# Performance work log

Measured on AMD Instinct MI355X. Metric: run time of the kernel, lower is better.

Reference implementation:

```python
import jax, jax.numpy as jnp
import numpy as np

N_NODES = 50000


def gcn_conv(x, src, dst, W, b, n_nodes):
    """PyG-style GCNConv: x' = D^-1/2 (A + I) D^-1/2 (x W) + b.
    src/dst already include self-loops."""
    h = x @ W  # [N, C_out]
    # symmetric normalization from degree (with self-loops, unit edge weight)
    deg = jax.ops.segment_sum(jnp.ones_like(dst, dtype=h.dtype), dst,
                              num_segments=n_nodes)  # [N]
    dinv = jnp.where(deg > 0, jax.lax.rsqrt(deg), 0.0)
    norm = dinv[src] * dinv[dst]  # [E]
    msg = h[src] * norm[:, None]  # gather + scale, [E, C_out]
    out = jax.ops.segment_sum(msg, dst, num_segments=n_nodes)  # scatter-add
    return out + b


def setup_inputs() -> dict:
    key = jax.random.key(0)
    k1, k2, k3, k4, k5, k6 = jax.random.split(key, 6)
    in_c, hid_c, out_c = 128, 64, 64
    x = jax.random.normal(k1, (N_NODES, in_c), dtype=jnp.float32)
    edge_index = jax.random.randint(k2, (2, 800000), 0, N_NODES, dtype=jnp.int64)
    # Glorot-ish init for weights, zeros for bias (as PyG default)
    W1 = jax.random.normal(k3, (in_c, hid_c), dtype=jnp.float32) / np.sqrt(in_c)
    b1 = jnp.zeros((hid_c,), dtype=jnp.float32)
    W2 = jax.random.normal(k4, (hid_c, out_c), dtype=jnp.float32) / np.sqrt(hid_c)
    b2 = jnp.zeros((out_c,), dtype=jnp.float32)
    return {"x": x, "edge_index": edge_index, "W1": W1, "b1": b1,
            "W2": W2, "b2": b2}


def reference(x, edge_index, W1, b1, W2, b2):
    n = x.shape[0]
    loops = jnp.arange(n, dtype=edge_index.dtype)
    src = jnp.concatenate([edge_index[0], loops])  # add self-loops
    dst = jnp.concatenate([edge_index[1], loops])
    h = gcn_conv(x, src, dst, W1, b1, n)
    h = jax.nn.relu(h)
    return gcn_conv(h, src, dst, W2, b2, n)
```

## Files before the change

kernel.cpp:

```cpp
#include <hip/hip_runtime.h>
#include <hip/hip_fp16.h>


#define C_HID 64
#define NCHUNK 512
#define ES3 1280
#define ES4 768

static inline size_t alignup(size_t x) { return (x + 255) & ~(size_t)255; }

typedef __attribute__((address_space(3))) unsigned int lds_uint;
typedef __attribute__((address_space(1))) const unsigned int glob_uint;

__device__ __forceinline__ int blockScanIncl256(int v, int* wsum) {
    const int lane = threadIdx.x & 63, wav = threadIdx.x >> 6;
    int s = v;
#pragma unroll
    for (int off = 1; off < 64; off <<= 1) {
        int t = __shfl_up(s, off);
        if (lane >= off) s += t;
    }
    if (lane == 63) wsum[wav] = s;
    __syncthreads();
    if (wav == 0 && lane < 4) {
        int ws = wsum[lane];
#pragma unroll
        for (int off = 1; off < 4; off <<= 1) {
            int t = __shfl_up(ws, off);
            if (lane >= off) ws += t;
        }
        wsum[lane] = ws;
    }
    __syncthreads();
    return (wav ? wsum[wav - 1] : 0) + s;
}

template <int K>
__global__ __launch_bounds__(256) void gemm1_hist_kernel(
    const float* __restrict__ X, const float* __restrict__ W,
    const int* __restrict__ dst, __half* __restrict__ outh,
    int* __restrict__ S, int n, int E, int ePer, int nb) {
    constexpr int KP = K + 4;
    __shared__ float Xs[64 * KP];
    __shared__ float Ws[K * 64];
    __shared__ int h[1024];
    const int t = threadIdx.x;
    const int lane = t & 63;
    const int wav = t >> 6;

    if ((int)blockIdx.x < NCHUNK) {
        for (int i = t; i < nb; i += 256) h[i] = 0;
        __syncthreads();
        int beg = blockIdx.x * ePer, end = min(E, beg + ePer);
        for (int e = beg + t; e < end; e += 256)
            atomicAdd(&h[dst[e] >> 6], 1);
        __syncthreads();
        for (int b = t; b < nb; b += 256)
            S[(size_t)b * NCHUNK + blockIdx.x] = h[b];
        return;
    }

    const int row0 = ((int)blockIdx.x - NCHUNK) * 64;
    {
        const char* gb = (const char*)W;
        char* lb = (char*)Ws;
        for (int off = wav * 1024; off < K * 64 * 4; off += 4096)
            __builtin_amdgcn_global_load_lds((glob_uint*)(gb + off + lane * 16),
                                             (lds_uint*)(lb + off), 16, 0, 0);
    }
    if (row0 + 64 <= n) {
        const float4* g4 = (const float4*)(X + (size_t)row0 * K);
        for (int i = t; i < 64 * (K / 4); i += 256) {
            float4 v = g4[i];
            int r = i / (K / 4), k0 = (i % (K / 4)) * 4;
            *(float4*)&Xs[r * KP + k0] = v;
        }
    } else {
        for (int i = t; i < 64 * K; i += 256) {
            int r = i / K, k = i % K;
            Xs[r * KP + k] = (row0 + r < n) ? X[(size_t)(row0 + r) * K + k] : 0.0f;
        }
    }
    __syncthreads();

    const int tx = t & 15;
    const int ty = t >> 4;
    float acc[4][4] = {{0.f}};
#pragma unroll 2
    for (int k0 = 0; k0 < K; k0 += 4) {
        float4 a0 = *(const float4*)&Xs[(4 * ty + 0) * KP + k0];
        float4 a1 = *(const float4*)&Xs[(4 * ty + 1) * KP + k0];
        float4 a2 = *(const float4*)&Xs[(4 * ty + 2) * KP + k0];
        float4 a3 = *(const float4*)&Xs[(4 * ty + 3) * KP + k0];
        float4 b0 = *(const float4*)&Ws[(k0 + 0) * 64 + 4 * tx];
        float4 b1 = *(const float4*)&Ws[(k0 + 1) * 64 + 4 * tx];
        float4 b2 = *(const float4*)&Ws[(k0 + 2) * 64 + 4 * tx];
        float4 b3 = *(const float4*)&Ws[(k0 + 3) * 64 + 4 * tx];
        const float* ap[4] = {(const float*)&a0, (const float*)&a1,
                              (const float*)&a2, (const float*)&a3};
        const float* bp[4] = {(const float*)&b0, (const float*)&b1,
                              (const float*)&b2, (const float*)&b3};
#pragma unroll
        for (int r = 0; r < 4; ++r)
#pragma unroll
            for (int kk = 0; kk < 4; ++kk) {
                float av = ap[r][kk];
#pragma unroll
                for (int c = 0; c < 4; ++c)
                    acc[r][c] = fmaf(av, bp[kk][c], acc[r][c]);
            }
    }
#pragma unroll
    for (int r = 0; r < 4; ++r) {
        int row = row0 + 4 * ty + r;
        if (row < n) {
            __half2 p01 = __floats2half2_rn(acc[r][0], acc[r][1]);
            __half2 p23 = __floats2half2_rn(acc[r][2], acc[r][3]);
            float2 st;
            ((__half2*)&st)[0] = p01;
            ((__half2*)&st)[1] = p23;
            *(float2*)&outh[(size_t)row * 64 + 4 * tx] = st;
        }
    }
}

__global__ __launch_bounds__(256) void scan_rows_kernel(
    int* __restrict__ S, int* __restrict__ T) {
    __shared__ int wsum[4];
    const int b = blockIdx.x, t = threadIdx.x;
    int4 v = make_int4(0, 0, 0, 0);
    if (t < NCHUNK / 4) v = ((const int4*)(S + (size_t)b * NCHUNK))[t];
    int p1 = v.x + v.y, p2 = p1 + v.z, p3 = p2 + v.w;
    int incl = blockScanIncl256(p3, wsum);
    int excl = incl - p3;
    if (t < NCHUNK / 4) {
        int4 o;
        o.x = excl; o.y = excl + v.x; o.z = excl + p1; o.w = excl + p2;
        ((int4*)(S + (size_t)b * NCHUNK))[t] = o;
    }
    if (t == 0) T[b] = wsum[3];
}

__global__ __launch_bounds__(256) void scatter_kernel(
    const int* __restrict__ src, const int* __restrict__ dst, int E, int ePer,
    const int* __restrict__ S, const int* __restrict__ T,
    unsigned* __restrict__ ebuf, int nb) {
    __shared__ int tmp[1024];
    __shared__ int arr[1024];
    __shared__ int wsum[4];
    const int b = blockIdx.x, t = threadIdx.x;
    {
        int a0 = (4 * t + 0 < nb) ? T[4 * t + 0] : 0;
        int a1 = (4 * t + 1 < nb) ? T[4 * t + 1] : 0;
        int a2 = (4 * t + 2 < nb) ? T[4 * t + 2] : 0;
        int a3 = (4 * t + 3 < nb) ? T[4 * t + 3] : 0;
        int p1 = a0 + a1, p2 = p1 + a2, p3 = p2 + a3;
        int incl = blockScanIncl256(p3, wsum);
        int excl = incl - p3;
        tmp[4 * t + 0] = excl;
        tmp[4 * t + 1] = excl + a0;
        tmp[4 * t + 2] = excl + p1;
        tmp[4 * t + 3] = excl + p2;
    }
    __syncthreads();
    for (int i = t; i < nb; i += 256)
        arr[i] = S[(size_t)i * NCHUNK + b] + tmp[i];
    __syncthreads();
    int beg = b * ePer, end = min(E, beg + ePer);
    for (int e = beg + t; e < end; e += 256) {
        int d = dst[e];
        int s = src[e];
        int pos = atomicAdd(&arr[d >> 6], 1);
        ebuf[pos] = ((unsigned)s << 6) | (unsigned)(d & 63);
    }
}

__global__ __launch_bounds__(256) void build_kernel(
    const unsigned* __restrict__ ebuf, const int* __restrict__ T,
    int* __restrict__ row_ptr, float* __restrict__ dinv,
    int* __restrict__ esrc, __half* __restrict__ g1, int n, int nb) {
    __shared__ int tmp[1024];
    __shared__ int cnt[64];
    __shared__ int cur[64];
    __shared__ float dvs[64];
    __shared__ int wsum[4];
    const int b = blockIdx.x, t = threadIdx.x;
    {
        int a0 = (4 * t + 0 < nb) ? T[4 * t + 0] : 0;
        int a1 = (4 * t + 1 < nb) ? T[4 * t + 1] : 0;
        int a2 = (4 * t + 2 < nb) ? T[4 * t + 2] : 0;
        int a3 = (4 * t + 3 < nb) ? T[4 * t + 3] : 0;
        int p1 = a0 + a1, p2 = p1 + a2, p3 = p2 + a3;
        int incl = blockScanIncl256(p3, wsum);
        int excl = incl - p3;
        tmp[4 * t + 0] = excl + a0;
        tmp[4 * t + 1] = excl + p1;
        tmp[4 * t + 2] = excl + p2;
        tmp[4 * t + 3] = excl + p3;
    }
    if (t < 64) cnt[t] = 0;
    __syncthreads();
    const int ebeg = b ? tmp[b - 1] : 0;
    const int eend = tmp[b];

    for (int e = ebeg + t; e < eend; e += 256)
        atomicAdd(&cnt[ebuf[e] & 63], 1);
    __syncthreads();
    if (t < 64) {
        int deg = cnt[t];
        int s = deg;
#pragma unroll
        for (int off = 1; off < 64; off <<= 1) {
            int x = __shfl_up(s, off);
            if (t >= off) s += x;
        }
        cur[t] = ebeg + s - deg;
        float dv = rsqrtf(1.0f + (float)deg);
        dvs[t] = dv;
        int v = (b << 6) + t;
        if (v < n) {
            row_ptr[v + 1] = ebeg + s;
            dinv[v] = dv;
            if (v == 0) row_ptr[0] = 0;
        }
    }
    __syncthreads();
    for (int e = ebeg + t; e < eend; e += 256) {
        unsigned p = ebuf[e];
        int pos = atomicAdd(&cur[p & 63], 1);
        esrc[pos] = (int)(p >> 6);
    }
    {
        const int row = t >> 2, q = t & 3;
        const int v = (b << 6) + row;
        if (v < n) {
            float dv = dvs[row];
            float4* gp = (float4*)(g1 + (size_t)v * 64 + q * 16);
            float4 r0 = gp[0], r1 = gp[1];
            __half2* h0 = (__half2*)&r0;
            __half2* h1 = (__half2*)&r1;
#pragma unroll
            for (int i2 = 0; i2 < 4; ++i2) {
                float2 f0 = __half22float2(h0[i2]);
                float2 f1 = __half22float2(h1[i2]);
                h0[i2] = __floats2half2_rn(f0.x * dv, f0.y * dv);
                h1[i2] = __floats2half2_rn(f1.x * dv, f1.y * dv);
            }
            gp[0] = r0;
            gp[1] = r1;
        }
    }
}

template <bool LDSE>
__device__ __forceinline__ void agg1_body(
    const float4* __restrict__ hs4, const int* es, const int* __restrict__ esg,
    int beg0, int beg, int end, int c, float acc[16]) {
    int j = beg;
    for (; j + 4 <= end; j += 4) {
        int s0, s1, s2, s3;
        if (LDSE) {
            s0 = es[j]; s1 = es[j + 1]; s2 = es[j + 2]; s3 = es[j + 3];
        } else {
            s0 = esg[beg0 + j]; s1 = esg[beg0 + j + 1];
            s2 = esg[beg0 + j + 2]; s3 = esg[beg0 + j + 3];
        }
        size_t rb0 = (size_t)s0 * 8 + 2 * c, rb1 = (size_t)s1 * 8 + 2 * c;
        size_t rb2 = (size_t)s2 * 8 + 2 * c, rb3 = (size_t)s3 * 8 + 2 * c;
        float4 a0 = hs4[rb0], a1 = hs4[rb0 + 1];
        float4 b0 = hs4[rb1], b1v = hs4[rb1 + 1];
        float4 c0 = hs4[rb2], c1 = hs4[rb2 + 1];
        float4 e0 = hs4[rb3], e1 = hs4[rb3 + 1];
        const __half2 *pa0 = (const __half2*)&a0, *pa1 = (const __half2*)&a1;
        const __half2 *pb0 = (const __half2*)&b0, *pb1 = (const __half2*)&b1v;
        const __half2 *pc0 = (const __half2*)&c0, *pc1 = (const __half2*)&c1;
        const __half2 *pe0 = (const __half2*)&e0, *pe1 = (const __half2*)&e1;
#pragma unroll
        for (int q = 0; q < 4; ++q) {
            float2 f;
            f = __half22float2(pa0[q]); acc[2 * q] += f.x; acc[2 * q + 1] += f.y;
            f = __half22float2(pa1[q]); acc[8 + 2 * q] += f.x; acc[9 + 2 * q] += f.y;
            f = __half22float2(pb0[q]); acc[2 * q] += f.x; acc[2 * q + 1] += f.y;
            f = __half22float2(pb1[q]); acc[8 + 2 * q] += f.x; acc[9 + 2 * q] += f.y;
            f = __half22float2(pc0[q]); acc[2 * q] += f.x; acc[2 * q + 1] += f.y;
            f = __half22float2(pc1[q]); acc[8 + 2 * q] += f.x; acc[9 + 2 * q] += f.y;
            f = __half22float2(pe0[q]); acc[2 * q] += f.x; acc[2 * q + 1] += f.y;
            f = __half22float2(pe1[q]); acc[8 + 2 * q] += f.x; acc[9 + 2 * q] += f.y;
        }
    }
    for (; j < end; ++j) {
        int s0 = LDSE ? es[j] : esg[beg0 + j];
        size_t rb0 = (size_t)s0 * 8 + 2 * c;
        float4 a0 = hs4[rb0], a1 = hs4[rb0 + 1];
        const __half2 *pa0 = (const __half2*)&a0, *pa1 = (const __half2*)&a1;
#pragma unroll
        for (int q = 0; q < 4; ++q) {
            float2 f;
            f = __half22float2(pa0[q]); acc[2 * q] += f.x; acc[2 * q + 1] += f.y;
            f = __half22float2(pa1[q]); acc[8 + 2 * q] += f.x; acc[9 + 2 * q] += f.y;
        }
    }
}

__global__ __launch_bounds__(256) void agg1_gemm2_kernel(
    const __half* __restrict__ g1, const int* __restrict__ row_ptr,
    const int* __restrict__ esrc, const float* __restrict__ dinv,
    const float* __restrict__ b1, const float* __restrict__ W2,
    __half* __restrict__ g2, int n) {
    __shared__ float Bt[64][68];
    __shared__ float Ws2[64 * 64];
    __shared__ int es[ES3];
    const int t = threadIdx.x, lane = t & 63, wav = t >> 6;
    const int row0 = blockIdx.x * 64;

    const int beg0 = row_ptr[row0];
    const int end0 = row_ptr[min(row0 + 64, n)];
    const int tot = end0 - beg0;
    const bool uselds = (tot <= ES3);
    if (uselds)
        for (int i = t; i < tot; i += 256) es[i] = esrc[beg0 + i];
    __syncthreads();

    {
        const char* gb = (const char*)W2;
        char* lb = (char*)Ws2;
        for (int off = wav * 1024; off < 64 * 64 * 4; off += 4096)
            __builtin_amdgcn_global_load_lds((glob_uint*)(gb + off + lane * 16),
                                             (lds_uint*)(lb + off), 16, 0, 0);
    }

    const int g = t >> 2;
    const int c = t & 3;
    const int v = row0 + g;
    const float4* __restrict__ hs4 = (const float4*)g1;

    if (v < n) {
        float acc[16];
        {
            size_t rb = (size_t)v * 8 + 2 * c;
            float4 r0 = hs4[rb], r1 = hs4[rb + 1];
            const __half2* h0 = (const __half2*)&r0;
            const __half2* h1 = (const __half2*)&r1;
#pragma unroll
            for (int q = 0; q < 4; ++q) {
                float2 f0 = __half22float2(h0[q]);
                float2 f1 = __half22float2(h1[q]);
                acc[2 * q] = f0.x;     acc[2 * q + 1] = f0.y;
                acc[8 + 2 * q] = f1.x; acc[9 + 2 * q] = f1.y;
            }
        }
        const int beg = row_ptr[v] - beg0;
        const int end = row_ptr[v + 1] - beg0;
        if (uselds) agg1_body<true>(hs4, es, esrc, beg0, beg, end, c, acc);
        else        agg1_body<false>(hs4, es, esrc, beg0, beg, end, c, acc);
        const float dv0 = dinv[v];
        const float* bb = b1 + c * 16;
#pragma unroll
        for (int u = 0; u < 4; ++u) {
            float4 w;
            w.x = fmaxf(fmaf(acc[4 * u + 0], dv0, bb[4 * u + 0]), 0.f);
            w.y = fmaxf(fmaf(acc[4 * u + 1], dv0, bb[4 * u + 1]), 0.f);
            w.z = fmaxf(fmaf(acc[4 * u + 2], dv0, bb[4 * u + 2]), 0.f);
            w.w = fmaxf(fmaf(acc[4 * u + 3], dv0, bb[4 * u + 3]), 0.f);
            *(float4*)&Bt[g][c * 16 + 4 * u] = w;
        }
    } else {
#pragma unroll
        for (int u = 0; u < 4; ++u)
            *(float4*)&Bt[g][c * 16 + 4 * u] = make_float4(0.f, 0.f, 0.f, 0.f);
    }
    __syncthreads();

    const int tx = t & 15;
    const int ty = t >> 4;
    float a2[4][4] = {{0.f}};
#pragma unroll 2
    for (int k0 = 0; k0 < 64; k0 += 4) {
        float4 x0 = *(const float4*)&Bt[4 * ty + 0][k0];
        float4 x1 = *(const float4*)&Bt[4 * ty + 1][k0];
        float4 x2 = *(const float4*)&Bt[4 * ty + 2][k0];
        float4 x3 = *(const float4*)&Bt[4 * ty + 3][k0];
        float4 w0 = *(const float4*)&Ws2[(k0 + 0) * 64 + 4 * tx];
        float4 w1 = *(const float4*)&Ws2[(k0 + 1) * 64 + 4 * tx];
        float4 w2 = *(const float4*)&Ws2[(k0 + 2) * 64 + 4 * tx];
        float4 w3 = *(const float4*)&Ws2[(k0 + 3) * 64 + 4 * tx];
        const float* xp[4] = {(const float*)&x0, (const float*)&x1,
                              (const float*)&x2, (const float*)&x3};
        const float* wp[4] = {(const float*)&w0, (const float*)&w1,
                              (const float*)&w2, (const float*)&w3};
#pragma unroll
        for (int r = 0; r < 4; ++r)
#pragma unroll
            for (int kk = 0; kk < 4; ++kk) {
                float av = xp[r][kk];
#pragma unroll
                for (int cc = 0; cc < 4; ++cc)
                    a2[r][cc] = fmaf(av, wp[kk][cc], a2[r][cc]);
            }
    }
#pragma unroll
    for (int r = 0; r < 4; ++r) {
        int row = row0 + 4 * ty + r;
        if (row < n) {
            float dv = dinv[row];
            __half2 p01 = __floats2half2_rn(a2[r][0] * dv, a2[r][1] * dv);
            __half2 p23 = __floats2half2_rn(a2[r][2] * dv, a2[r][3] * dv);
            float2 st;
            ((__half2*)&st)[0] = p01;
            ((__half2*)&st)[1] = p23;
            *(float2*)&g2[(size_t)row * 64 + 4 * tx] = st;
        }
    }
}

template <bool LDSE>
__device__ __forceinline__ void agg2_body(
    const float4* __restrict__ hs4, const int* es, const int* __restrict__ esg,
    int beg0, int beg, int end, int c8, float acc[8]) {
    int j = beg;
    for (; j + 4 <= end; j += 4) {
        int s0, s1, s2, s3;
        if (LDSE) {
            s0 = es[j]; s1 = es[j + 1]; s2 = es[j + 2]; s3 = es[j + 3];
        } else {
            s0 = esg[beg0 + j]; s1 = esg[beg0 + j + 1];
            s2 = esg[beg0 + j + 2]; s3 = esg[beg0 + j + 3];
        }
        float4 r0 = hs4[(size_t)s0 * 8 + c8];
        float4 r1 = hs4[(size_t)s1 * 8 + c8];
        float4 r2 = hs4[(size_t)s2 * 8 + c8];
        float4 r3 = hs4[(size_t)s3 * 8 + c8];
        const __half2* h0 = (const __half2*)&r0;
        const __half2* h1 = (const __half2*)&r1;
        const __half2* h2 = (const __half2*)&r2;
        const __half2* h3 = (const __half2*)&r3;
#pragma unroll
        for (int q = 0; q < 4; ++q) {
            float2 f0 = __half22float2(h0[q]);
            float2 f1 = __half22float2(h1[q]);
            float2 f2 = __half22float2(h2[q]);
            float2 f3 = __half22float2(h3[q]);
            acc[2 * q]     += (f0.x + f1.x) + (f2.x + f3.x);
            acc[2 * q + 1] += (f0.y + f1.y) + (f2.y + f3.y);
        }
    }
    for (; j < end; ++j) {
        int s0 = LDSE ? es[j] : esg[beg0 + j];
        float4 r0 = hs4[(size_t)s0 * 8 + c8];
        const __half2* h0 = (const __half2*)&r0;
#pragma unroll
        for (int q = 0; q < 4; ++q) {
            float2 f0 = __half22float2(h0[q]);
            acc[2 * q] += f0.x;
            acc[2 * q + 1] += f0.y;
        }
    }
}

__global__ __launch_bounds__(256) void aggregate2_kernel(
    const __half* __restrict__ hs,
    const int* __restrict__ row_ptr,
    const int* __restrict__ esrc,
    const float* __restrict__ dinv,
    const float* __restrict__ bias,
    float* __restrict__ out, int n) {
    __shared__ int es[ES4];
    const int t = threadIdx.x;
    const int row0 = blockIdx.x * 32;
    const int beg0 = row_ptr[row0];
    const int end0 = row_ptr[min(row0 + 32, n)];
    const int tot = end0 - beg0;
    const bool uselds = (tot <= ES4);
    if (uselds)
        for (int i = t; i < tot; i += 256) es[i] = esrc[beg0 + i];
    __syncthreads();

    const int v = row0 + (t >> 3);
    if (v >= n) return;
    const int c8 = t & 7;
    const float4* __restrict__ hs4 = (const float4*)hs;

    float acc[8];
    {
        float4 raw = hs4[(size_t)v * 8 + c8];
        const __half2* hp = (const __half2*)&raw;
#pragma unroll
        for (int q = 0; q < 4; ++q) {
            float2 f = __half22float2(hp[q]);
            acc[2 * q] = f.x; acc[2 * q + 1] = f.y;
        }
    }

    const int beg = row_ptr[v] - beg0;
    const int end = row_ptr[v + 1] - beg0;
    if (uselds) agg2_body<true>(hs4, es, esrc, beg0, beg, end, c8, acc);
    else        agg2_body<false>(hs4, es, esrc, beg0, beg, end, c8, acc);

    float dv = dinv[v];
    float4 b0 = *(const float4*)(bias + c8 * 8);
    float4 b1v = *(const float4*)(bias + c8 * 8 + 4);
    float4 o0, o1;
    o0.x = fmaf(acc[0], dv, b0.x); o0.y = fmaf(acc[1], dv, b0.y);
    o0.z = fmaf(acc[2], dv, b0.z); o0.w = fmaf(acc[3], dv, b0.w);
    o1.x = fmaf(acc[4], dv, b1v.x); o1.y = fmaf(acc[5], dv, b1v.y);
    o1.z = fmaf(acc[6], dv, b1v.z); o1.w = fmaf(acc[7], dv, b1v.w);
    float4* op = (float4*)(out + (size_t)v * 64 + c8 * 8);
    op[0] = o0;
    op[1] = o1;
}

extern "C" void kernel_launch(void* const* d_in, const int* in_sizes, int n_in,
                              void* d_out, int out_size, void* d_ws, size_t ws_size,
                              hipStream_t stream) {
    const float* x  = (const float*)d_in[0];
    const int*   ei = (const int*)d_in[1];
    const float* W1 = (const float*)d_in[2];
    const float* b1 = (const float*)d_in[3];
    const float* W2 = (const float*)d_in[4];
    const float* b2 = (const float*)d_in[5];
    float* out = (float*)d_out;

    const int C_IN = 128;
    const int n = in_sizes[0] / C_IN;
    const int E = in_sizes[1] / 2;
    const int* src = ei;
    const int* dst = ei + E;

    const int nb = (n + 63) >> 6;
    const int ngb = (n + 63) / 64;
    const int ePer = (E + NCHUNK - 1) / NCHUNK;

    char* w = (char*)d_ws;
    float*    dinv    = (float*)w;    w += alignup((size_t)n * sizeof(float));
    __half*   g1      = (__half*)w;   w += alignup((size_t)n * C_HID * sizeof(__half));
    __half*   g2      = (__half*)w;   w += alignup((size_t)n * C_HID * sizeof(__half));
    int*      row_ptr = (int*)w;      w += alignup((size_t)(n + 1) * sizeof(int));
    int*      S       = (int*)w;      w += alignup((size_t)nb * NCHUNK * sizeof(int));
    int*      T       = (int*)w;      w += alignup((size_t)(nb + 1) * sizeof(int));
    unsigned* ebuf    = (unsigned*)w; w += alignup((size_t)E * sizeof(unsigned));
    int*      esrc    = (int*)w;

    gemm1_hist_kernel<128><<<NCHUNK + ngb, 256, 0, stream>>>(
        x, W1, dst, g1, S, n, E, ePer, nb);

    scan_rows_kernel<<<nb, 256, 0, stream>>>(S, T);
    scatter_kernel<<<NCHUNK, 256, 0, stream>>>(src, dst, E, ePer, S, T, ebuf, nb);
    build_kernel<<<nb, 256, 0, stream>>>(ebuf, T, row_ptr, dinv, esrc, g1, n, nb);

    agg1_gemm2_kernel<<<ngb, 256, 0, stream>>>(
        g1, row_ptr, esrc, dinv, b1, W2, g2, n);

    aggregate2_kernel<<<(n + 31) / 32, 256, 0, stream>>>(
        g2, row_ptr, esrc, dinv, b2, out, n);
}
```

Baseline: 163.9 us.

## Use 8 lanes per node in agg1 with 32-row blocks and shared 8-wide gather

The first aggregation+GEMM kernel now handles 32 nodes per block with 8 threads per node, each loading one float4 (8 halves) per neighbor instead of 4 threads loading two float4s. A unified gather body unrolled by 8 edges serves both aggregation kernels, giving more loads in flight per thread. The intent is more parallelism and memory-level concurrency for the irregular gather, at the cost of recomputing the W2 LDS load over twice as many blocks and a smaller per-block GEMM tile.

```diff
diff --git a/kernel.cpp b/kernel.cpp
--- a/kernel.cpp
+++ b/kernel.cpp
@@ -4,7 +4,7 @@
 
 #define C_HID 64
 #define NCHUNK 512
-#define ES3 1280
+#define ES3 768
 #define ES4 768
 
 static inline size_t alignup(size_t x) { return (x + 255) & ~(size_t)255; }
@@ -252,53 +252,61 @@
     }
 }
 
+__device__ __forceinline__ void addf4(float acc[8], const float4& r) {
+    const __half2* h = (const __half2*)&r;
+#pragma unroll
+    for (int q = 0; q < 4; ++q) {
+        float2 f = __half22float2(h[q]);
+        acc[2 * q] += f.x;
+        acc[2 * q + 1] += f.y;
+    }
+}
+
 template <bool LDSE>
-__device__ __forceinline__ void agg1_body(
+__device__ __forceinline__ void agg8_body(
     const float4* __restrict__ hs4, const int* es, const int* __restrict__ esg,
-    int beg0, int beg, int end, int c, float acc[16]) {
+    int beg0, int beg, int end, int c8, float acc[8]) {
     int j = beg;
-    for (; j + 4 <= end; j += 4) {
+    for (; j + 8 <= end; j += 8) {
+        int s0, s1, s2, s3, s4, s5, s6, s7;
+        if (LDSE) {
+            s0 = es[j];     s1 = es[j + 1]; s2 = es[j + 2]; s3 = es[j + 3];
+            s4 = es[j + 4]; s5 = es[j + 5]; s6 = es[j + 6]; s7 = es[j + 7];
+        } else {
+            const int* p = esg + beg0 + j;
+            s0 = p[0]; s1 = p[1]; s2 = p[2]; s3 = p[3];
+            s4 = p[4]; s5 = p[5]; s6 = p[6]; s7 = p[7];
+        }
+        float4 r0 = hs4[(size_t)s0 * 8 + c8];
+        float4 r1 = hs4[(size_t)s1 * 8 + c8];
+        float4 r2 = hs4[(size_t)s2 * 8 + c8];
+        float4 r3 = hs4[(size_t)s3 * 8 + c8];
+        float4 r4 = hs4[(size_t)s4 * 8 + c8];
+        float4 r5 = hs4[(size_t)s5 * 8 + c8];
+        float4 r6 = hs4[(size_t)s6 * 8 + c8];
+        float4 r7 = hs4[(size_t)s7 * 8 + c8];
+        addf4(acc, r0); addf4(acc, r1); addf4(acc, r2); addf4(acc, r3);
+        addf4(acc, r4); addf4(acc, r5); addf4(acc, r6); addf4(acc, r7);
+    }
+    if (j + 4 <= end) {
         int s0, s1, s2, s3;
         if (LDSE) {
             s0 = es[j]; s1 = es[j + 1]; s2 = es[j + 2]; s3 = es[j + 3];
         } else {
-            s0 = esg[beg0 + j]; s1 = esg[beg0 + j + 1];
-            s2 = esg[beg0 + j + 2]; s3 = esg[beg0 + j + 3];
-        }
-        size_t rb0 = (size_t)s0 * 8 + 2 * c, rb1 = (size_t)s1 * 8 + 2 * c;
-        size_t rb2 = (size_t)s2 * 8 + 2 * c, rb3 = (size_t)s3 * 8 + 2 * c;
-        float4 a0 = hs4[rb0], a1 = hs4[rb0 + 1];
-        float4 b0 = hs4[rb1], b1v = hs4[rb1 + 1];
-        float4 c0 = hs4[rb2], c1 = hs4[rb2 + 1];
-        float4 e0 = hs4[rb3], e1 = hs4[rb3 + 1];
-        const __half2 *pa0 = (const __half2*)&a0, *pa1 = (const __half2*)&a1;
-        const __half2 *pb0 = (const __half2*)&b0, *pb1 = (const __half2*)&b1v;
-        const __half2 *pc0 = (const __half2*)&c0, *pc1 = (const __half2*)&c1;
-        const __half2 *pe0 = (const __half2*)&e0, *pe1 = (const __half2*)&e1;
-#pragma unroll
-        for (int q = 0; q < 4; ++q) {
-            float2 f;
-            f = __half22float2(pa0[q]); acc[2 * q] += f.x; acc[2 * q + 1] += f.y;
-            f = __half22float2(pa1[q]); acc[8 + 2 * q] += f.x; acc[9 + 2 * q] += f.y;
-            f = __half22float2(pb0[q]); acc[2 * q] += f.x; acc[2 * q + 1] += f.y;
-            f = __half22float2(pb1[q]); acc[8 + 2 * q] += f.x; acc[9 + 2 * q] += f.y;
-            f = __half22float2(pc0[q]); acc[2 * q] += f.x; acc[2 * q + 1] += f.y;
-            f = __half22float2(pc1[q]); acc[8 + 2 * q] += f.x; acc[9 + 2 * q] += f.y;
-            f = __half22float2(pe0[q]); acc[2 * q] += f.x; acc[2 * q + 1] += f.y;
-            f = __half22float2(pe1[q]); acc[8 + 2 * q] += f.x; acc[9 + 2 * q] += f.y;
-        }
+            const int* p = esg + beg0 + j;
+            s0 = p[0]; s1 = p[1]; s2 = p[2]; s3 = p[3];
+        }
+        float4 r0 = hs4[(size_t)s0 * 8 + c8];
+        float4 r1 = hs4[(size_t)s1 * 8 + c8];
+        float4 r2 = hs4[(size_t)s2 * 8 + c8];
+        float4 r3 = hs4[(size_t)s3 * 8 + c8];
+        addf4(acc, r0); addf4(acc, r1); addf4(acc, r2); addf4(acc, r3);
+        j += 4;
     }
     for (; j < end; ++j) {
         int s0 = LDSE ? es[j] : esg[beg0 + j];
-        size_t rb0 = (size_t)s0 * 8 + 2 * c;
-        float4 a0 = hs4[rb0], a1 = hs4[rb0 + 1];
-        const __half2 *pa0 = (const __half2*)&a0, *pa1 = (const __half2*)&a1;
-#pragma unroll
-        for (int q = 0; q < 4; ++q) {
-            float2 f;
-            f = __half22float2(pa0[q]); acc[2 * q] += f.x; acc[2 * q + 1] += f.y;
-            f = __half22float2(pa1[q]); acc[8 + 2 * q] += f.x; acc[9 + 2 * q] += f.y;
-        }
+        float4 r0 = hs4[(size_t)s0 * 8 + c8];
+        addf4(acc, r0);
     }
 }
 
@@ -307,14 +315,14 @@
     const int* __restrict__ esrc, const float* __restrict__ dinv,
     const float* __restrict__ b1, const float* __restrict__ W2,
     __half* __restrict__ g2, int n) {
-    __shared__ float Bt[64][68];
+    __shared__ float Bt[32][68];
     __shared__ float Ws2[64 * 64];
     __shared__ int es[ES3];
     const int t = threadIdx.x, lane = t & 63, wav = t >> 6;
-    const int row0 = blockIdx.x * 64;
+    const int row0 = blockIdx.x * 32;
 
     const int beg0 = row_ptr[row0];
-    const int end0 = row_ptr[min(row0 + 64, n)];
+    const int end0 = row_ptr[min(row0 + 32, n)];
     const int tot = end0 - beg0;
     const bool uselds = (tot <= ES3);
     if (uselds)
@@ -329,67 +337,61 @@
                                              (lds_uint*)(lb + off), 16, 0, 0);
     }
 
-    const int g = t >> 2;
-    const int c = t & 3;
+    const int g = t >> 3;
+    const int c8 = t & 7;
     const int v = row0 + g;
     const float4* __restrict__ hs4 = (const float4*)g1;
 
     if (v < n) {
-        float acc[16];
+        float acc[8];
         {
-            size_t rb = (size_t)v * 8 + 2 * c;
-            float4 r0 = hs4[rb], r1 = hs4[rb + 1];
-            const __half2* h0 = (const __half2*)&r0;
-            const __half2* h1 = (const __half2*)&r1;
+            float4 raw = hs4[(size_t)v * 8 + c8];
+            const __half2* hp = (const __half2*)&raw;
 #pragma unroll
             for (int q = 0; q < 4; ++q) {
-                float2 f0 = __half22float2(h0[q]);
-                float2 f1 = __half22float2(h1[q]);
-                acc[2 * q] = f0.x;     acc[2 * q + 1] = f0.y;
-                acc[8 + 2 * q] = f1.x; acc[9 + 2 * q] = f1.y;
+                float2 f = __half22float2(hp[q]);
+                acc[2 * q] = f.x; acc[2 * q + 1] = f.y;
             }
         }
         const int beg = row_ptr[v] - beg0;
         const int end = row_ptr[v + 1] - beg0;
-        if (uselds) agg1_body<true>(hs4, es, esrc, beg0, beg, end, c, acc);
-        else        agg1_body<false>(hs4, es, esrc, beg0, beg, end, c, acc);
+        if (uselds) agg8_body<true>(hs4, es, esrc, beg0, beg, end, c8, acc);
+        else        agg8_body<false>(hs4, es, esrc, beg0, beg, end, c8, acc);
         const float dv0 = dinv[v];
-        const float* bb = b1 + c * 16;
-#pragma unroll
-        for (int u = 0; u < 4; ++u) {
-            float4 w;
-            w.x = fmaxf(fmaf(acc[4 * u + 0], dv0, bb[4 * u + 0]), 0.f);
-            w.y = fmaxf(fmaf(acc[4 * u + 1], dv0, bb[4 * u + 1]), 0.f);
-            w.z = fmaxf(fmaf(acc[4 * u + 2], dv0, bb[4 * u + 2]), 0.f);
-            w.w = fmaxf(fmaf(acc[4 * u + 3], dv0, bb[4 * u + 3]), 0.f);
-            *(float4*)&Bt[g][c * 16 + 4 * u] = w;
-        }
+        const float* bb = b1 + c8 * 8;
+        float4 w0, w1;
+        w0.x = fmaxf(fmaf(acc[0], dv0, bb[0]), 0.f);
+        w0.y = fmaxf(fmaf(acc[1], dv0, bb[1]), 0.f);
+        w0.z = fmaxf(fmaf(acc[2], dv0, bb[2]), 0.f);
+        w0.w = fmaxf(fmaf(acc[3], dv0, bb[3]), 0.f);
+        w1.x = fmaxf(fmaf(acc[4], dv0, bb[4]), 0.f);
+        w1.y = fmaxf(fmaf(acc[5], dv0, bb[5]), 0.f);
+        w1.z = fmaxf(fmaf(acc[6], dv0, bb[6]), 0.f);
+        w1.w = fmaxf(fmaf(acc[7], dv0, bb[7]), 0.f);
+        *(float4*)&Bt[g][c8 * 8] = w0;
+        *(float4*)&Bt[g][c8 * 8 + 4] = w1;
     } else {
-#pragma unroll
-        for (int u = 0; u < 4; ++u)
-            *(float4*)&Bt[g][c * 16 + 4 * u] = make_float4(0.f, 0.f, 0.f, 0.f);
+        *(float4*)&Bt[g][c8 * 8] = make_float4(0.f, 0.f, 0.f, 0.f);
+        *(float4*)&Bt[g][c8 * 8 + 4] = make_float4(0.f, 0.f, 0.f, 0.f);
     }
     __syncthreads();
 
     const int tx = t & 15;
     const int ty = t >> 4;
-    float a2[4][4] = {{0.f}};
+    float a2[2][4] = {{0.f}};
 #pragma unroll 2
     for (int k0 = 0; k0 < 64; k0 += 4) {
-        float4 x0 = *(const float4*)&Bt[4 * ty + 0][k0];
-        float4 x1 = *(const float4*)&Bt[4 * ty + 1][k0];
-        float4 x2 = *(const float4*)&Bt[4 * ty + 2][k0];
-        float4 x3 = *(const float4*)&Bt[4 * ty + 3][k0];
+        float4 x0 = *(const float4*)&Bt[2 * ty + 0][k0];
+        float4 x1 = *(const float4*)&Bt[2 * ty + 1][k0];
         float4 w0 = *(const float4*)&Ws2[(k0 + 0) * 64 + 4 * tx];
         float4 w1 = *(const float4*)&Ws2[(k0 + 1) * 64 + 4 * tx];
         float4 w2 = *(const float4*)&Ws2[(k0 + 2) * 64 + 4 * tx];
         float4 w3 = *(const float4*)&Ws2[(k0 + 3) * 64 + 4 * tx];
-        const float* xp[4] = {(const float*)&x0, (const float*)&x1,
-                              (const float*)&x2, (const float*)&x3};
+        const float* xp[2] = {(const float*)&x0, (const float*)&x1};
         const float* wp[4] = {(const float*)&w0, (const float*)&w1,
                               (const float*)&w2, (const float*)&w3};
 #pragma unroll
-        for (int r = 0; r < 4; ++r)
+        for (int r = 0; r < 2; ++r)
 #pragma unroll
             for (int kk = 0; kk < 4; ++kk) {
                 float av = xp[r][kk];
@@ -399,8 +401,8 @@
             }
     }
 #pragma unroll
-    for (int r = 0; r < 4; ++r) {
-        int row = row0 + 4 * ty + r;
+    for (int r = 0; r < 2; ++r) {
+        int row = row0 + 2 * ty + r;
         if (row < n) {
             float dv = dinv[row];
             __half2 p01 = __floats2half2_rn(a2[r][0] * dv, a2[r][1] * dv);
@@ -409,50 +411,6 @@
             ((__half2*)&st)[0] = p01;
             ((__half2*)&st)[1] = p23;
             *(float2*)&g2[(size_t)row * 64 + 4 * tx] = st;
-        }
-    }
-}
-
-template <bool LDSE>
-__device__ __forceinline__ void agg2_body(
-    const float4* __restrict__ hs4, const int* es, const int* __restrict__ esg,
-    int beg0, int beg, int end, int c8, float acc[8]) {
-    int j = beg;
-    for (; j + 4 <= end; j += 4) {
-        int s0, s1, s2, s3;
-        if (LDSE) {
-            s0 = es[j]; s1 = es[j + 1]; s2 = es[j + 2]; s3 = es[j + 3];
-        } else {
-            s0 = esg[beg0 + j]; s1 = esg[beg0 + j + 1];
-            s2 = esg[beg0 + j + 2]; s3 = esg[beg0 + j + 3];
-        }
-        float4 r0 = hs4[(size_t)s0 * 8 + c8];
-        float4 r1 = hs4[(size_t)s1 * 8 + c8];
-        float4 r2 = hs4[(size_t)s2 * 8 + c8];
-        float4 r3 = hs4[(size_t)s3 * 8 + c8];
-        const __half2* h0 = (const __half2*)&r0;
-        const __half2* h1 = (const __half2*)&r1;
-        const __half2* h2 = (const __half2*)&r2;
-        const __half2* h3 = (const __half2*)&r3;
-#pragma unroll
-        for (int q = 0; q < 4; ++q) {
-            float2 f0 = __half22float2(h0[q]);
-            float2 f1 = __half22float2(h1[q]);
-            float2 f2 = __half22float2(h2[q]);
-            float2 f3 = __half22float2(h3[q]);
-            acc[2 * q]     += (f0.x + f1.x) + (f2.x + f3.x);
-            acc[2 * q + 1] += (f0.y + f1.y) + (f2.y + f3.y);
-        }
-    }
-    for (; j < end; ++j) {
-        int s0 = LDSE ? es[j] : esg[beg0 + j];
-        float4 r0 = hs4[(size_t)s0 * 8 + c8];
-        const __half2* h0 = (const __half2*)&r0;
-#pragma unroll
-        for (int q = 0; q < 4; ++q) {
-            float2 f0 = __half22float2(h0[q]);
-            acc[2 * q] += f0.x;
-            acc[2 * q + 1] += f0.y;
         }
     }
 }
@@ -493,8 +451,8 @@
 
     const int beg = row_ptr[v] - beg0;
     const int end = row_ptr[v + 1] - beg0;
-    if (uselds) agg2_body<true>(hs4, es, esrc, beg0, beg, end, c8, acc);
-    else        agg2_body<false>(hs4, es, esrc, beg0, beg, end, c8, acc);
+    if (uselds) agg8_body<true>(hs4, es, esrc, beg0, beg, end, c8, acc);
+    else        agg8_body<false>(hs4, es, esrc, beg0, beg, end, c8, acc);
 
     float dv = dinv[v];
     float4 b0 = *(const float4*)(bias + c8 * 8);
@@ -528,6 +486,7 @@
 
     const int nb = (n + 63) >> 6;
     const int ngb = (n + 63) / 64;
+    const int n32 = (n + 31) / 32;
     const int ePer = (E + NCHUNK - 1) / NCHUNK;
 
     char* w = (char*)d_ws;
@@ -547,9 +506,9 @@
     scatter_kernel<<<NCHUNK, 256, 0, stream>>>(src, dst, E, ePer, S, T, ebuf, nb);
     build_kernel<<<nb, 256, 0, stream>>>(ebuf, T, row_ptr, dinv, esrc, g1, n, nb);
 
-    agg1_gemm2_kernel<<<ngb, 256, 0, stream>>>(
+    agg1_gemm2_kernel<<<n32, 256, 0, stream>>>(
         g1, row_ptr, esrc, dinv, b1, W2, g2, n);
 
-    aggregate2_kernel<<<(n + 31) / 32, 256, 0, stream>>>(
+    aggregate2_kernel<<<n32, 256, 0, stream>>>(
         g2, row_ptr, esrc, dinv, b2, out, n);
 }
```

Measured after the change: 161.2 us. No clear change (-1.6%).
